# Performance work log

Measured on AMD Instinct MI355X. Metric: run time of the kernel, lower is better.

Reference implementation:

```python
import jax, jax.numpy as jnp
import numpy as np

PI = float(np.pi)

def _quantize_angle(theta):
    deg = theta * (180.0 / PI)
    deg = jnp.where(deg < 0, deg + 180.0, deg)
    q = jnp.round(deg / 45.0) * 45.0
    # 180 is treated the same as 0 in the original branch (theta==0 or theta==180)
    return jnp.where(q == 180.0, 0.0, q)

def setup_inputs() -> dict:
    key = jax.random.key(0)
    k1, k2 = jax.random.split(key)
    H, W = 4096, 4096
    img = jax.random.uniform(k1, (1, 1, H, W), dtype=jnp.float32)
    theta = jax.random.normal(k2, (1, 1, H, W), dtype=jnp.float32)  # radians
    return {"img": img, "theta": theta}

def reference(img, theta):
    q = _quantize_angle(theta)

    # value of neighbor at (x+dx, y+dy); borders are masked out afterwards so
    # roll wrap-around never affects the result (interior pixels only).
    def nbr(dx, dy):
        return jnp.roll(img, shift=(-dx, -dy), axis=(2, 3))

    def local_max(dx, dy):
        return (img >= nbr(dx, dy)) & (img >= nbr(-dx, -dy))

    m0 = local_max(0, 1)     # theta == 0 / 180: compare (x, y+-1)
    m45 = local_max(1, 1)    # theta == 45:      compare (x+-1, y+-1)
    m90 = local_max(1, 0)    # theta == 90:      compare (x+-1, y)
    m135 = local_max(1, -1)  # theta == 135:     compare (x+1,y-1),(x-1,y+1)

    mask = jnp.where(q == 0.0, m0,
           jnp.where(q == 45.0, m45,
           jnp.where(q == 90.0, m90, m135)))

    H, W = img.shape[2], img.shape[3]
    interior = jnp.zeros((H, W), dtype=bool).at[1:-1, 1:-1].set(True)
    return jnp.where(mask & interior, img, jnp.zeros_like(img))
```

## Files before the change

kernel.cpp:

```cpp
#include <hip/hip_runtime.h>
#include <math.h>

#define IMG_H 4096
#define IMG_W 4096
#define ROWS_PER_THREAD 8

__global__ __launch_bounds__(256) void nms_kernel(const float* __restrict__ img,
                                                  const float* __restrict__ theta,
                                                  float* __restrict__ out) {
    const int tid = blockIdx.x * blockDim.x + threadIdx.x;
    const int g  = tid >> 10;
    const int qc = tid & 1023;
    const int y4 = qc << 2;
    const int x0 = g * ROWS_PER_THREAD;

    const int yl = (y4 > 0)         ? y4 - 1 : 0;
    const int yr = (y4 + 4 < IMG_W) ? y4 + 4 : IMG_W - 1;

    auto load_row = [&](int x, float4& v, float& el, float& er) {
        const float* row = img + (long long)x * IMG_W;
        v  = *(const float4*)(row + y4);
        el = row[yl];
        er = row[yr];
    };

    float4 u, c, d;
    float ul, ur, cl, cr, dl, dr;

    const int xu0 = (x0 > 0) ? x0 - 1 : 0;
    load_row(xu0, u, ul, ur);
    load_row(x0,  c, cl, cr);

    #pragma unroll
    for (int i = 0; i < ROWS_PER_THREAD; ++i) {
        const int x  = x0 + i;
        const int xd = (x < IMG_H - 1) ? x + 1 : IMG_H - 1;
        load_row(xd, d, dl, dr);

        const long long base = (long long)x * IMG_W + y4;
        const float4 th = *(const float4*)(theta + base);

        const float cv[6] = {cl, c.x, c.y, c.z, c.w, cr};
        const float uv[6] = {ul, u.x, u.y, u.z, u.w, ur};
        const float dv[6] = {dl, d.x, d.y, d.z, d.w, dr};
        const float tv[4] = {th.x, th.y, th.z, th.w};

        const bool row_interior = (x > 0) && (x < IMG_H - 1);
        float ov[4];

        #pragma unroll
        for (int j = 0; j < 4; ++j) {
            const float v = cv[j + 1];

            float deg = tv[j] * 57.29577951308232f;
            if (deg < 0.0f) deg += 180.0f;
            float q = rintf(deg / 45.0f) * 45.0f;
            if (q == 180.0f) q = 0.0f;

            float a, b;
            if (q == 0.0f) {
                a = cv[j + 2]; b = cv[j];
            } else if (q == 45.0f) {
                a = dv[j + 2]; b = uv[j];
            } else if (q == 90.0f) {
                a = dv[j + 1]; b = uv[j + 1];
            } else {
                a = dv[j]; b = uv[j + 2];
            }

            const int y = y4 + j;
            const bool interior = row_interior && (y > 0) && (y < IMG_W - 1);
            ov[j] = ((v >= a) && (v >= b) && interior) ? v : 0.0f;
        }

        float4 o;
        o.x = ov[0]; o.y = ov[1]; o.z = ov[2]; o.w = ov[3];
        *(float4*)(out + base) = o;

        u = c; ul = cl; ur = cr;
        c = d; cl = dl; cr = dr;
    }
}

extern "C" void kernel_launch(void* const* d_in, const int* in_sizes, int n_in,
                              void* d_out, int out_size, void* d_ws, size_t ws_size,
                              hipStream_t stream) {
    const float* img   = (const float*)d_in[0];
    const float* theta = (const float*)d_in[1];
    float* out = (float*)d_out;

    const int total_threads = (IMG_H / ROWS_PER_THREAD) * (IMG_W / 4);
    const int block = 256;
    const int grid = total_threads / block;
    nms_kernel<<<grid, block, 0, stream>>>(img, theta, out);
}
```

Baseline: 175.6 us.

## Halve rows per thread and make direction selection branchless per pixel

New measurement: 170.4 us. 1.03x faster.

```diff
diff --git a/kernel.cpp b/kernel.cpp
--- a/kernel.cpp
+++ b/kernel.cpp
@@ -3,78 +3,70 @@
 
 #define IMG_H 4096
 #define IMG_W 4096
-#define ROWS_PER_THREAD 8
+#define RPT 4
+
+__device__ __forceinline__ float nms_px(float t, bool interior,
+                                        float uL, float uC, float uR,
+                                        float cL, float cC, float cR,
+                                        float dL, float dC, float dR) {
+    float deg = t * 57.29577951308232f;
+    deg = (deg < 0.0f) ? deg + 180.0f : deg;
+    float q = rintf(deg / 45.0f) * 45.0f;
+    const bool is0  = (q == 0.0f) || (q == 180.0f);
+    const bool is45 = (q == 45.0f);
+    const bool is90 = (q == 90.0f);
+    const float a = is0 ? cR : (is45 ? dR : (is90 ? dC : dL));
+    const float b = is0 ? cL : (is45 ? uL : (is90 ? uC : uR));
+    return ((cC >= a) && (cC >= b) && interior) ? cC : 0.0f;
+}
 
 __global__ __launch_bounds__(256) void nms_kernel(const float* __restrict__ img,
                                                   const float* __restrict__ theta,
                                                   float* __restrict__ out) {
     const int tid = blockIdx.x * blockDim.x + threadIdx.x;
     const int g  = tid >> 10;
-    const int qc = tid & 1023;
-    const int y4 = qc << 2;
-    const int x0 = g * ROWS_PER_THREAD;
+    const int y4 = (tid & 1023) << 2;
+    const int x0 = g * RPT;
 
     const int yl = (y4 > 0)         ? y4 - 1 : 0;
     const int yr = (y4 + 4 < IMG_W) ? y4 + 4 : IMG_W - 1;
 
-    auto load_row = [&](int x, float4& v, float& el, float& er) {
-        const float* row = img + (long long)x * IMG_W;
-        v  = *(const float4*)(row + y4);
-        el = row[yl];
-        er = row[yr];
-    };
+    const bool col0_int = (y4 > 0);
+    const bool col3_int = (y4 + 4 < IMG_W);
 
     float4 u, c, d;
     float ul, ur, cl, cr, dl, dr;
 
-    const int xu0 = (x0 > 0) ? x0 - 1 : 0;
-    load_row(xu0, u, ul, ur);
-    load_row(x0,  c, cl, cr);
+    {
+        const int xu0 = (x0 > 0) ? x0 - 1 : 0;
+        const float* __restrict__ pr = img + (size_t)xu0 * IMG_W;
+        u = *(const float4*)(pr + y4); ul = pr[yl]; ur = pr[yr];
+    }
+    {
+        const float* __restrict__ pr = img + (size_t)x0 * IMG_W;
+        c = *(const float4*)(pr + y4); cl = pr[yl]; cr = pr[yr];
+    }
 
     #pragma unroll
-    for (int i = 0; i < ROWS_PER_THREAD; ++i) {
+    for (int i = 0; i < RPT; ++i) {
         const int x  = x0 + i;
         const int xd = (x < IMG_H - 1) ? x + 1 : IMG_H - 1;
-        load_row(xd, d, dl, dr);
+        {
+            const float* __restrict__ pr = img + (size_t)xd * IMG_W;
+            d = *(const float4*)(pr + y4); dl = pr[yl]; dr = pr[yr];
+        }
 
-        const long long base = (long long)x * IMG_W + y4;
+        const size_t base = (size_t)x * IMG_W + y4;
         const float4 th = *(const float4*)(theta + base);
 
-        const float cv[6] = {cl, c.x, c.y, c.z, c.w, cr};
-        const float uv[6] = {ul, u.x, u.y, u.z, u.w, ur};
-        const float dv[6] = {dl, d.x, d.y, d.z, d.w, dr};
-        const float tv[4] = {th.x, th.y, th.z, th.w};
-
-        const bool row_interior = (x > 0) && (x < IMG_H - 1);
-        float ov[4];
-
-        #pragma unroll
-        for (int j = 0; j < 4; ++j) {
-            const float v = cv[j + 1];
-
-            float deg = tv[j] * 57.29577951308232f;
-            if (deg < 0.0f) deg += 180.0f;
-            float q = rintf(deg / 45.0f) * 45.0f;
-            if (q == 180.0f) q = 0.0f;
-
-            float a, b;
-            if (q == 0.0f) {
-                a = cv[j + 2]; b = cv[j];
-            } else if (q == 45.0f) {
-                a = dv[j + 2]; b = uv[j];
-            } else if (q == 90.0f) {
-                a = dv[j + 1]; b = uv[j + 1];
-            } else {
-                a = dv[j]; b = uv[j + 2];
-            }
-
-            const int y = y4 + j;
-            const bool interior = row_interior && (y > 0) && (y < IMG_W - 1);
-            ov[j] = ((v >= a) && (v >= b) && interior) ? v : 0.0f;
-        }
+        const bool row_int = (x > 0) && (x < IMG_H - 1);
 
         float4 o;
-        o.x = ov[0]; o.y = ov[1]; o.z = ov[2]; o.w = ov[3];
+        o.x = nms_px(th.x, row_int && col0_int, ul,  u.x, u.y,  cl,  c.x, c.y,  dl,  d.x, d.y);
+        o.y = nms_px(th.y, row_int,             u.x, u.y, u.z,  c.x, c.y, c.z,  d.x, d.y, d.z);
+        o.z = nms_px(th.z, row_int,             u.y, u.z, u.w,  c.y, c.z, c.w,  d.y, d.z, d.w);
+        o.w = nms_px(th.w, row_int && col3_int, u.z, u.w, ur,   c.z, c.w, cr,   d.z, d.w, dr);
+
         *(float4*)(out + base) = o;
 
         u = c; ul = cl; ur = cr;
@@ -89,7 +81,7 @@
     const float* theta = (const float*)d_in[1];
     float* out = (float*)d_out;
 
-    const int total_threads = (IMG_H / ROWS_PER_THREAD) * (IMG_W / 4);
+    const int total_threads = (IMG_H / RPT) * (IMG_W / 4);
     const int block = 256;
     const int grid = total_threads / block;
     nms_kernel<<<grid, block, 0, stream>>>(img, theta, out);
```
